# Kernel optimization log

Hardware: AMD Instinct MI355X
Metric: run time of the kernel (lower is better)

Reference implementation:

```python
import jax, jax.numpy as jnp
import numpy as np

TAU = 0.5
EPS = 1e-8
NEG = -1e30  # masked logit value (finite to keep grads clean)

B, L1, L2 = 8, 2048, 2048


def setup_inputs() -> dict:
    key = jax.random.key(0)
    k1, k2 = jax.random.split(key)
    sim_matrix = jax.random.normal(k1, (B, L1, L2), dtype=jnp.float32)
    # per-sample valid lengths in [1024, 2048] so masking is exercised but no row is empty
    lengths = jax.random.randint(k2, (B, 2), 1024, 2049, dtype=jnp.int32)
    return {"sim_matrix": sim_matrix, "lengths": lengths}


def reference(sim_matrix, lengths):
    # mask[b,i,j] = (i < lengths[b,0]) & (j < lengths[b,1])
    i_idx = jnp.arange(sim_matrix.shape[1])[None, :, None]
    j_idx = jnp.arange(sim_matrix.shape[2])[None, None, :]
    mask = (i_idx < lengths[:, 0, None, None]) & (j_idx < lengths[:, 1, None, None])

    logits = jnp.where(mask, sim_matrix / TAU, NEG)
    row_sm = jax.nn.softmax(logits, axis=-1)   # competition over L2 per row
    col_sm = jax.nn.softmax(logits, axis=-2)   # competition over L1 per column

    # geometric mean of the two assignments; zero outside valid region
    out = jnp.where(mask, jnp.sqrt(EPS + row_sm * col_sm), 0.0)
    return out
```

## Files before the change

kernel.cpp:

```cpp
#include <hip/hip_runtime.h>
#include <math.h>

#define L 2048
#define BATCH 8
#define RPS 16
#define NSPLIT (L / RPS)
#define EPSF 1e-8f
#define C2 2.885390081777927f
#define C4 5.770780163555854f

typedef float f32x4 __attribute__((ext_vector_type(4)));

__device__ __forceinline__ float fexp2(float x) {
  return __builtin_amdgcn_exp2f(x);
}
__device__ __forceinline__ float fsqrt(float x) {
  return __builtin_amdgcn_sqrtf(x);
}

__global__ __launch_bounds__(256) void stats_k(
    const float* __restrict__ sim, const int* __restrict__ lengths,
    float* __restrict__ rinv, float* __restrict__ pcol) {
  const int b = blockIdx.y;
  const int islab = blockIdx.x;
  const int len0 = lengths[2 * b], len1 = lengths[2 * b + 1];
  const int tid = threadIdx.x;
  const int wave = tid >> 6, lane = tid & 63;
  const int i0 = islab * RPS + wave * 4;
  const int jb = lane * 4;
  const int nrow = min(4, len0 - i0);

  float4 cacc[8];
#pragma unroll
  for (int s = 0; s < 8; ++s) cacc[s] = make_float4(0.f, 0.f, 0.f, 0.f);
  float racc[4] = {0.f, 0.f, 0.f, 0.f};

#pragma unroll
  for (int r = 0; r < 4; ++r) {
    if (r < nrow) {
      const float* p = sim + ((size_t)b * L + (i0 + r)) * L + jb;
      float acc = 0.f;
#pragma unroll
      for (int s = 0; s < 8; ++s) {
        float4 v = *reinterpret_cast<const float4*>(p + s * 256);
        float4 e;
        e.x = fexp2(v.x * C2); e.y = fexp2(v.y * C2);
        e.z = fexp2(v.z * C2); e.w = fexp2(v.w * C2);
        if (s >= 4) {
          const int j = s * 256 + jb;
          if (j + 0 >= len1) e.x = 0.f;
          if (j + 1 >= len1) e.y = 0.f;
          if (j + 2 >= len1) e.z = 0.f;
          if (j + 3 >= len1) e.w = 0.f;
        }
        acc += (e.x + e.y) + (e.z + e.w);
        cacc[s].x += e.x; cacc[s].y += e.y; cacc[s].z += e.z; cacc[s].w += e.w;
      }
      racc[r] = acc;
    }
  }

#pragma unroll
  for (int r = 0; r < 4; ++r) {
    if (r < nrow) {
      float v = racc[r];
#pragma unroll
      for (int off = 1; off < 64; off <<= 1) v += __shfl_xor(v, off, 64);
      if (lane == 0) rinv[(size_t)b * L + (i0 + r)] = 1.0f / v;
    }
  }

  __shared__ float cpart[4][2048];
#pragma unroll
  for (int s = 0; s < 8; ++s)
    *reinterpret_cast<float4*>(&cpart[wave][s * 256 + jb]) = cacc[s];
  __syncthreads();

#pragma unroll
  for (int h = 0; h < 2; ++h) {
    const int c = h * 1024 + tid * 4;
    float4 a0 = *reinterpret_cast<const float4*>(&cpart[0][c]);
    float4 a1 = *reinterpret_cast<const float4*>(&cpart[1][c]);
    float4 a2 = *reinterpret_cast<const float4*>(&cpart[2][c]);
    float4 a3 = *reinterpret_cast<const float4*>(&cpart[3][c]);
    f32x4 o;
    o.x = (a0.x + a1.x) + (a2.x + a3.x);
    o.y = (a0.y + a1.y) + (a2.y + a3.y);
    o.z = (a0.z + a1.z) + (a2.z + a3.z);
    o.w = (a0.w + a1.w) + (a2.w + a3.w);
    __builtin_nontemporal_store(
        o, reinterpret_cast<f32x4*>(&pcol[(size_t)(b * NSPLIT + islab) * L + c]));
  }
}

__global__ __launch_bounds__(128) void col_merge_k(
    const float* __restrict__ pcol, float* __restrict__ cinv) {
  const int idx = blockIdx.x * 128 + threadIdx.x;
  const int b = idx >> 11, j = idx & (L - 1);
  const float* p = pcol + (size_t)b * NSPLIT * L + j;
  float s = 0.f;
#pragma unroll 16
  for (int c = 0; c < NSPLIT; ++c)
    s += __builtin_nontemporal_load(p + (size_t)c * L);
  cinv[idx] = 1.0f / s;
}

__global__ __launch_bounds__(512) void finalize_k(
    const float* __restrict__ sim, const int* __restrict__ lengths,
    const float* __restrict__ rinv, const float* __restrict__ cinv,
    float* __restrict__ out) {
  const int row = blockIdx.x;
  const int b = row >> 11, i = row & (L - 1);
  const int len0 = lengths[2 * b], len1 = lengths[2 * b + 1];
  const int j = threadIdx.x * 4;
  const size_t off = (size_t)row * L + j;
  f32x4 o;
  if (i >= len0) {
    o = (f32x4){0.f, 0.f, 0.f, 0.f};
  } else {
    const float ri = rinv[row];
    f32x4 v = __builtin_nontemporal_load(
        reinterpret_cast<const f32x4*>(sim + off));
    f32x4 ci = *reinterpret_cast<const f32x4*>(cinv + ((size_t)b << 11) + j);
    o.x = (j + 0 < len1) ? fsqrt(EPSF + fexp2(v.x * C4) * ri * ci.x) : 0.f;
    o.y = (j + 1 < len1) ? fsqrt(EPSF + fexp2(v.y * C4) * ri * ci.y) : 0.f;
    o.z = (j + 2 < len1) ? fsqrt(EPSF + fexp2(v.z * C4) * ri * ci.z) : 0.f;
    o.w = (j + 3 < len1) ? fsqrt(EPSF + fexp2(v.w * C4) * ri * ci.w) : 0.f;
  }
  __builtin_nontemporal_store(o, reinterpret_cast<f32x4*>(out + off));
}

extern "C" void kernel_launch(void* const* d_in, const int* in_sizes, int n_in,
                              void* d_out, int out_size, void* d_ws, size_t ws_size,
                              hipStream_t stream) {
  const float* sim = (const float*)d_in[0];
  const int* lengths = (const int*)d_in[1];
  float* out = (float*)d_out;
  float* ws = (float*)d_ws;

  const int NR = BATCH * L;
  float* rinv = ws;
  float* cinv = ws + NR;
  float* pcol = ws + 2 * (size_t)NR;

  hipLaunchKernelGGL(stats_k, dim3(NSPLIT, BATCH), dim3(256), 0, stream,
                     sim, lengths, rinv, pcol);
  hipLaunchKernelGGL(col_merge_k, dim3(NR / 128), dim3(128), 0, stream,
                     pcol, cinv);
  hipLaunchKernelGGL(finalize_k, dim3(NR), dim3(512), 0, stream,
                     sim, lengths, rinv, cinv, out);
}
```

Baseline: 248.1 us.

## Fuse stats, column merge and finalize into one cooperative kernel with grid syncs

Replaces the three-kernel pipeline with a single cooperative kernel of 512 blocks. Each block handles 32 rows, keeps its row reciprocals in registers, and writes column partials. A grid sync precedes a distributed column merge, and a second grid sync precedes the output pass, which rereads sim (ideally hitting cache) and uses cinv staged in LDS. This removes the launch gaps and the rinv round trip but adds grid-wide barrier cost and lowers parallelism to 512 blocks. The old three-kernel path remains as a fallback if the cooperative launch fails.

Measured after the change: 366.7 us. +47.8%, slower.

```diff
diff --git a/kernel.cpp b/kernel.cpp
--- a/kernel.cpp
+++ b/kernel.cpp
@@ -1,8 +1,13 @@
 #include <hip/hip_runtime.h>
+#include <hip/hip_cooperative_groups.h>
 #include <math.h>
+
+namespace cg = cooperative_groups;
 
 #define L 2048
 #define BATCH 8
+#define NS2 64
+#define GRID2 (BATCH * NS2)
 #define RPS 16
 #define NSPLIT (L / RPS)
 #define EPSF 1e-8f
@@ -18,27 +23,31 @@
   return __builtin_amdgcn_sqrtf(x);
 }
 
-__global__ __launch_bounds__(256) void stats_k(
+__global__ __launch_bounds__(256, 2) void fused_k(
     const float* __restrict__ sim, const int* __restrict__ lengths,
-    float* __restrict__ rinv, float* __restrict__ pcol) {
-  const int b = blockIdx.y;
-  const int islab = blockIdx.x;
+    float* __restrict__ pcol, float* __restrict__ cinv,
+    float* __restrict__ out) {
+  const int bid = blockIdx.x;
+  const int b = bid >> 6;
+  const int sb = bid & 63;
   const int len0 = lengths[2 * b], len1 = lengths[2 * b + 1];
   const int tid = threadIdx.x;
   const int wave = tid >> 6, lane = tid & 63;
-  const int i0 = islab * RPS + wave * 4;
+  const int i0w = sb * 32 + wave * 8;
   const int jb = lane * 4;
-  const int nrow = min(4, len0 - i0);
+  const int nrow = min(8, len0 - i0w);
+
+  __shared__ float cpart[4][2048];
 
   float4 cacc[8];
 #pragma unroll
   for (int s = 0; s < 8; ++s) cacc[s] = make_float4(0.f, 0.f, 0.f, 0.f);
-  float racc[4] = {0.f, 0.f, 0.f, 0.f};
-
-#pragma unroll
-  for (int r = 0; r < 4; ++r) {
+  float racc[8] = {0.f, 0.f, 0.f, 0.f, 0.f, 0.f, 0.f, 0.f};
+
+#pragma unroll
+  for (int r = 0; r < 8; ++r) {
     if (r < nrow) {
-      const float* p = sim + ((size_t)b * L + (i0 + r)) * L + jb;
+      const float* p = sim + ((size_t)b * L + (i0w + r)) * L + jb;
       float acc = 0.f;
 #pragma unroll
       for (int s = 0; s < 8; ++s) {
@@ -60,17 +69,15 @@
     }
   }
 
-#pragma unroll
-  for (int r = 0; r < 4; ++r) {
-    if (r < nrow) {
-      float v = racc[r];
-#pragma unroll
-      for (int off = 1; off < 64; off <<= 1) v += __shfl_xor(v, off, 64);
-      if (lane == 0) rinv[(size_t)b * L + (i0 + r)] = 1.0f / v;
-    }
-  }
-
-  __shared__ float cpart[4][2048];
+  float rinv_r[8];
+#pragma unroll
+  for (int r = 0; r < 8; ++r) {
+    float v = racc[r];
+#pragma unroll
+    for (int off = 1; off < 64; off <<= 1) v += __shfl_xor(v, off, 64);
+    rinv_r[r] = 1.0f / v;
+  }
+
 #pragma unroll
   for (int s = 0; s < 8; ++s)
     *reinterpret_cast<float4*>(&cpart[wave][s * 256 + jb]) = cacc[s];
@@ -83,13 +90,149 @@
     float4 a1 = *reinterpret_cast<const float4*>(&cpart[1][c]);
     float4 a2 = *reinterpret_cast<const float4*>(&cpart[2][c]);
     float4 a3 = *reinterpret_cast<const float4*>(&cpart[3][c]);
-    f32x4 o;
+    float4 o;
     o.x = (a0.x + a1.x) + (a2.x + a3.x);
     o.y = (a0.y + a1.y) + (a2.y + a3.y);
     o.z = (a0.z + a1.z) + (a2.z + a3.z);
     o.w = (a0.w + a1.w) + (a2.w + a3.w);
-    __builtin_nontemporal_store(
-        o, reinterpret_cast<f32x4*>(&pcol[(size_t)(b * NSPLIT + islab) * L + c]));
+    *reinterpret_cast<float4*>(&pcol[(size_t)(b * NS2 + sb) * L + c]) = o;
+  }
+
+  cg::this_grid().sync();
+
+  {
+    const int colbase = bid * 32;
+    const int b2 = colbase >> 11;
+    const int j2 = (colbase & (L - 1)) + (tid & 31);
+    const int g = tid >> 5;
+    const float* p = pcol + ((size_t)b2 * NS2 + g * 8) * L + j2;
+    float s = 0.f;
+#pragma unroll
+    for (int c = 0; c < 8; ++c) s += p[(size_t)c * L];
+    cpart[0][tid] = s;
+    __syncthreads();
+    if (tid < 32) {
+      float t = 0.f;
+#pragma unroll
+      for (int gg = 0; gg < 8; ++gg) t += cpart[0][gg * 32 + tid];
+      cinv[colbase + tid] = 1.0f / t;
+    }
+  }
+
+  cg::this_grid().sync();
+
+#pragma unroll
+  for (int q = 0; q < 2; ++q)
+    cpart[0][q * 1024 + tid * 4 + 0 + 0] = 0.f;
+  {
+#pragma unroll
+    for (int q = 0; q < 2; ++q) {
+      const int c = q * 1024 + tid * 4;
+      *reinterpret_cast<float4*>(&cpart[0][c]) =
+          *reinterpret_cast<const float4*>(cinv + (b << 11) + c);
+    }
+  }
+  __syncthreads();
+
+#pragma unroll
+  for (int r = 0; r < 8; ++r) {
+    const int i = i0w + r;
+    const size_t off = ((size_t)b * L + i) * L + jb;
+    if (r < nrow) {
+      const float ri = rinv_r[r];
+#pragma unroll
+      for (int s = 0; s < 8; ++s) {
+        const int j = s * 256 + jb;
+        f32x4 v = *reinterpret_cast<const f32x4*>(sim + off + s * 256);
+        float4 ci = *reinterpret_cast<const float4*>(&cpart[0][j]);
+        f32x4 o;
+        o.x = (j + 0 < len1) ? fsqrt(EPSF + fexp2(v.x * C4) * ri * ci.x) : 0.f;
+        o.y = (j + 1 < len1) ? fsqrt(EPSF + fexp2(v.y * C4) * ri * ci.y) : 0.f;
+        o.z = (j + 2 < len1) ? fsqrt(EPSF + fexp2(v.z * C4) * ri * ci.z) : 0.f;
+        o.w = (j + 3 < len1) ? fsqrt(EPSF + fexp2(v.w * C4) * ri * ci.w) : 0.f;
+        __builtin_nontemporal_store(
+            o, reinterpret_cast<f32x4*>(out + off + s * 256));
+      }
+    } else {
+      const f32x4 z = (f32x4){0.f, 0.f, 0.f, 0.f};
+#pragma unroll
+      for (int s = 0; s < 8; ++s)
+        __builtin_nontemporal_store(
+            z, reinterpret_cast<f32x4*>(out + off + s * 256));
+    }
+  }
+}
+
+__global__ __launch_bounds__(256) void stats_k(
+    const float* __restrict__ sim, const int* __restrict__ lengths,
+    float* __restrict__ rinv, float* __restrict__ pcol) {
+  const int b = blockIdx.y;
+  const int islab = blockIdx.x;
+  const int len0 = lengths[2 * b], len1 = lengths[2 * b + 1];
+  const int tid = threadIdx.x;
+  const int wave = tid >> 6, lane = tid & 63;
+  const int i0 = islab * RPS + wave * 4;
+  const int jb = lane * 4;
+  const int nrow = min(4, len0 - i0);
+
+  float4 cacc[8];
+#pragma unroll
+  for (int s = 0; s < 8; ++s) cacc[s] = make_float4(0.f, 0.f, 0.f, 0.f);
+  float racc[4] = {0.f, 0.f, 0.f, 0.f};
+
+#pragma unroll
+  for (int r = 0; r < 4; ++r) {
+    if (r < nrow) {
+      const float* p = sim + ((size_t)b * L + (i0 + r)) * L + jb;
+      float acc = 0.f;
+#pragma unroll
+      for (int s = 0; s < 8; ++s) {
+        float4 v = *reinterpret_cast<const float4*>(p + s * 256);
+        float4 e;
+        e.x = fexp2(v.x * C2); e.y = fexp2(v.y * C2);
+        e.z = fexp2(v.z * C2); e.w = fexp2(v.w * C2);
+        if (s >= 4) {
+          const int j = s * 256 + jb;
+          if (j + 0 >= len1) e.x = 0.f;
+          if (j + 1 >= len1) e.y = 0.f;
+          if (j + 2 >= len1) e.z = 0.f;
+          if (j + 3 >= len1) e.w = 0.f;
+        }
+        acc += (e.x + e.y) + (e.z + e.w);
+        cacc[s].x += e.x; cacc[s].y += e.y; cacc[s].z += e.z; cacc[s].w += e.w;
+      }
+      racc[r] = acc;
+    }
+  }
+#pragma unroll
+  for (int r = 0; r < 4; ++r) {
+    if (r < nrow) {
+      float v = racc[r];
+#pragma unroll
+      for (int off = 1; off < 64; off <<= 1) v += __shfl_xor(v, off, 64);
+      if (lane == 0) rinv[(size_t)b * L + (i0 + r)] = 1.0f / v;
+    }
+  }
+
+  __shared__ float cpart[4][2048];
+#pragma unroll
+  for (int s = 0; s < 8; ++s)
+    *reinterpret_cast<float4*>(&cpart[wave][s * 256 + jb]) = cacc[s];
+  __syncthreads();
+
+#pragma unroll
+  for (int h = 0; h < 2; ++h) {
+    const int c = h * 1024 + tid * 4;
+    float4 a0 = *reinterpret_cast<const float4*>(&cpart[0][c]);
+    float4 a1 = *reinterpret_cast<const float4*>(&cpart[1][c]);
+    float4 a2 = *reinterpret_cast<const float4*>(&cpart[2][c]);
+    float4 a3 = *reinterpret_cast<const float4*>(&cpart[3][c]);
+    float4 o;
+    o.x = (a0.x + a1.x) + (a2.x + a3.x);
+    o.y = (a0.y + a1.y) + (a2.y + a3.y);
+    o.z = (a0.z + a1.z) + (a2.z + a3.z);
+    o.w = (a0.w + a1.w) + (a2.w + a3.w);
+    *reinterpret_cast<float4*>(&pcol[(size_t)(b * NSPLIT + islab) * L + c]) = o;
   }
 }
 
@@ -100,8 +243,7 @@
   const float* p = pcol + (size_t)b * NSPLIT * L + j;
   float s = 0.f;
 #pragma unroll 16
-  for (int c = 0; c < NSPLIT; ++c)
-    s += __builtin_nontemporal_load(p + (size_t)c * L);
+  for (int c = 0; c < NSPLIT; ++c) s += p[(size_t)c * L];
   cinv[idx] = 1.0f / s;
 }
 
@@ -143,10 +285,16 @@
   float* cinv = ws + NR;
   float* pcol = ws + 2 * (size_t)NR;
 
-  hipLaunchKernelGGL(stats_k, dim3(NSPLIT, BATCH), dim3(256), 0, stream,
-                     sim, lengths, rinv, pcol);
-  hipLaunchKernelGGL(col_merge_k, dim3(NR / 128), dim3(128), 0, stream,
-                     pcol, cinv);
-  hipLaunchKernelGGL(finalize_k, dim3(NR), dim3(512), 0, stream,
-                     sim, lengths, rinv, cinv, out);
-}
+  void* args[] = {(void*)&sim, (void*)&lengths, (void*)&pcol,
+                  (void*)&cinv, (void*)&out};
+  hipError_t err = hipLaunchCooperativeKernel(
+      (const void*)fused_k, dim3(GRID2), dim3(256), args, 0, stream);
+  if (err != hipSuccess) {
+    hipLaunchKernelGGL(stats_k, dim3(NSPLIT, BATCH), dim3(256), 0, stream,
+                       sim, lengths, rinv, pcol);
+    hipLaunchKernelGGL(col_merge_k, dim3(NR / 128), dim3(128), 0, stream,
+                       pcol, cinv);
+    hipLaunchKernelGGL(finalize_k, dim3(NR), dim3(512), 0, stream,
+                       sim, lengths, rinv, cinv, out);
+  }
+}
```

## Replace partial column-sum buffer and merge kernel with global atomic accumulation

Applied to the files above, without the earlier changes.

The per-slab partial column sums are now added into a zeroed global column-sum buffer with float atomicAdd instead of being written to a large buffer and reduced by a separate merge kernel. Finalize computes the reciprocal of each column sum on the fly with the hardware rcp. This removes the 8 MB partial-sum write and read and one kernel launch, at the cost of an extra zeroing kernel, 128-way atomic contention per column, and nondeterministic summation order. The shuffle reduction is also made unconditional so all lanes take part.

After: 248.1 us. No clear change (+0.0%).

```diff
diff --git a/kernel.cpp b/kernel.cpp
--- a/kernel.cpp
+++ b/kernel.cpp
@@ -17,10 +17,18 @@
 __device__ __forceinline__ float fsqrt(float x) {
   return __builtin_amdgcn_sqrtf(x);
 }
+__device__ __forceinline__ float frcp(float x) {
+  return __builtin_amdgcn_rcpf(x);
+}
+
+__global__ __launch_bounds__(512) void zero_k(float* __restrict__ colsum) {
+  const int i = (blockIdx.x * 512 + threadIdx.x) * 4;
+  *reinterpret_cast<f32x4*>(colsum + i) = (f32x4){0.f, 0.f, 0.f, 0.f};
+}
 
 __global__ __launch_bounds__(256) void stats_k(
     const float* __restrict__ sim, const int* __restrict__ lengths,
-    float* __restrict__ rinv, float* __restrict__ pcol) {
+    float* __restrict__ rinv, float* __restrict__ colsum) {
   const int b = blockIdx.y;
   const int islab = blockIdx.x;
   const int len0 = lengths[2 * b], len1 = lengths[2 * b + 1];
@@ -62,12 +70,10 @@
 
 #pragma unroll
   for (int r = 0; r < 4; ++r) {
-    if (r < nrow) {
-      float v = racc[r];
+    float v = racc[r];
 #pragma unroll
-      for (int off = 1; off < 64; off <<= 1) v += __shfl_xor(v, off, 64);
-      if (lane == 0) rinv[(size_t)b * L + (i0 + r)] = 1.0f / v;
-    }
+    for (int off = 1; off < 64; off <<= 1) v += __shfl_xor(v, off, 64);
+    if (lane == 0 && r < nrow) rinv[(size_t)b * L + (i0 + r)] = 1.0f / v;
   }
 
   __shared__ float cpart[4][2048];
@@ -76,6 +82,7 @@
     *reinterpret_cast<float4*>(&cpart[wave][s * 256 + jb]) = cacc[s];
   __syncthreads();
 
+  float* cbase = colsum + ((size_t)b << 11);
 #pragma unroll
   for (int h = 0; h < 2; ++h) {
     const int c = h * 1024 + tid * 4;
@@ -83,31 +90,16 @@
     float4 a1 = *reinterpret_cast<const float4*>(&cpart[1][c]);
     float4 a2 = *reinterpret_cast<const float4*>(&cpart[2][c]);
     float4 a3 = *reinterpret_cast<const float4*>(&cpart[3][c]);
-    f32x4 o;
-    o.x = (a0.x + a1.x) + (a2.x + a3.x);
-    o.y = (a0.y + a1.y) + (a2.y + a3.y);
-    o.z = (a0.z + a1.z) + (a2.z + a3.z);
-    o.w = (a0.w + a1.w) + (a2.w + a3.w);
-    __builtin_nontemporal_store(
-        o, reinterpret_cast<f32x4*>(&pcol[(size_t)(b * NSPLIT + islab) * L + c]));
+    atomicAdd(cbase + c + 0, (a0.x + a1.x) + (a2.x + a3.x));
+    atomicAdd(cbase + c + 1, (a0.y + a1.y) + (a2.y + a3.y));
+    atomicAdd(cbase + c + 2, (a0.z + a1.z) + (a2.z + a3.z));
+    atomicAdd(cbase + c + 3, (a0.w + a1.w) + (a2.w + a3.w));
   }
-}
-
-__global__ __launch_bounds__(128) void col_merge_k(
-    const float* __restrict__ pcol, float* __restrict__ cinv) {
-  const int idx = blockIdx.x * 128 + threadIdx.x;
-  const int b = idx >> 11, j = idx & (L - 1);
-  const float* p = pcol + (size_t)b * NSPLIT * L + j;
-  float s = 0.f;
-#pragma unroll 16
-  for (int c = 0; c < NSPLIT; ++c)
-    s += __builtin_nontemporal_load(p + (size_t)c * L);
-  cinv[idx] = 1.0f / s;
 }
 
 __global__ __launch_bounds__(512) void finalize_k(
     const float* __restrict__ sim, const int* __restrict__ lengths,
-    const float* __restrict__ rinv, const float* __restrict__ cinv,
+    const float* __restrict__ rinv, const float* __restrict__ colsum,
     float* __restrict__ out) {
   const int row = blockIdx.x;
   const int b = row >> 11, i = row & (L - 1);
@@ -121,7 +113,10 @@
     const float ri = rinv[row];
     f32x4 v = __builtin_nontemporal_load(
         reinterpret_cast<const f32x4*>(sim + off));
-    f32x4 ci = *reinterpret_cast<const f32x4*>(cinv + ((size_t)b << 11) + j);
+    f32x4 cs = *reinterpret_cast<const f32x4*>(colsum + ((size_t)b << 11) + j);
+    f32x4 ci;
+    ci.x = frcp(cs.x); ci.y = frcp(cs.y);
+    ci.z = frcp(cs.z); ci.w = frcp(cs.w);
     o.x = (j + 0 < len1) ? fsqrt(EPSF + fexp2(v.x * C4) * ri * ci.x) : 0.f;
     o.y = (j + 1 < len1) ? fsqrt(EPSF + fexp2(v.y * C4) * ri * ci.y) : 0.f;
     o.z = (j + 2 < len1) ? fsqrt(EPSF + fexp2(v.z * C4) * ri * ci.z) : 0.f;
@@ -140,13 +135,11 @@
 
   const int NR = BATCH * L;
   float* rinv = ws;
-  float* cinv = ws + NR;
-  float* pcol = ws + 2 * (size_t)NR;
+  float* colsum = ws + NR;
 
+  hipLaunchKernelGGL(zero_k, dim3(NR / 2048), dim3(512), 0, stream, colsum);
   hipLaunchKernelGGL(stats_k, dim3(NSPLIT, BATCH), dim3(256), 0, stream,
-                     sim, lengths, rinv, pcol);
-  hipLaunchKernelGGL(col_merge_k, dim3(NR / 128), dim3(128), 0, stream,
-                     pcol, cinv);
+                     sim, lengths, rinv, colsum);
   hipLaunchKernelGGL(finalize_k, dim3(NR), dim3(512), 0, stream,
-                     sim, lengths, rinv, cinv, out);
+                     sim, lengths, rinv, colsum, out);
 }
```
